# Kernel tuning notes

Measured on AMD Instinct MI355X. Metric: run time of the kernel, lower is better.

Reference implementation:

```python
import jax, jax.numpy as jnp
import numpy as np

B, P, H, D = 32, 384, 384, 512
DA, DC, DH, NUM_LABELS = 512, 512, 512, 3


def setup_inputs() -> dict:
    key = jax.random.key(0)
    ks = jax.random.split(key, 12)
    s = lambda d: 1.0 / np.sqrt(d)
    return {
        "embedded_premise": jax.random.normal(ks[0], (B, P, D), jnp.float32),
        "embedded_hypothesis": jax.random.normal(ks[1], (B, H, D), jnp.float32),
        "premise_mask": jax.random.randint(ks[2], (B, P), 0, 2, jnp.int32),
        "hypothesis_mask": jax.random.randint(ks[3], (B, H), 0, 2, jnp.int32),
        "W_attend": jax.random.normal(ks[4], (D, DA), jnp.float32) * s(D),
        "b_attend": jnp.zeros((DA,), jnp.float32),
        "W_compare": jax.random.normal(ks[5], (2 * D, DC), jnp.float32) * s(2 * D),
        "b_compare": jnp.zeros((DC,), jnp.float32),
        "W_agg1": jax.random.normal(ks[6], (2 * DC, DH), jnp.float32) * s(2 * DC),
        "b_agg1": jnp.zeros((DH,), jnp.float32),
        "W_agg2": jax.random.normal(ks[7], (DH, NUM_LABELS), jnp.float32) * s(DH),
        "b_agg2": jnp.zeros((NUM_LABELS,), jnp.float32),
    }


def masked_softmax(scores, mask):
    # AllenNLP (legacy, non-memory-efficient) masked_softmax:
    # softmax(scores * mask), re-mask, renormalize with epsilon.
    result = jax.nn.softmax(scores * mask, axis=-1)
    result = result * mask
    return result / (jnp.sum(result, axis=-1, keepdims=True) + 1e-13)


def reference(embedded_premise, embedded_hypothesis, premise_mask, hypothesis_mask,
              W_attend, b_attend, W_compare, b_compare,
              W_agg1, b_agg1, W_agg2, b_agg2):
    pm = premise_mask.astype(jnp.float32)      # [B, P]
    hm = hypothesis_mask.astype(jnp.float32)   # [B, H]

    # TimeDistributed attend feedforward (shared weights)
    proj_p = jax.nn.relu(embedded_premise @ W_attend + b_attend)      # [B, P, DA]
    proj_h = jax.nn.relu(embedded_hypothesis @ W_attend + b_attend)   # [B, H, DA]

    # Dot-product similarity matrix [B, P, H]
    sim = jnp.einsum('bpd,bhd->bph', proj_p, proj_h)

    # Cross attention with masked softmax
    p2h = masked_softmax(sim, hm[:, None, :])                          # [B, P, H]
    attended_hypothesis = jnp.einsum('bph,bhd->bpd', p2h, embedded_hypothesis)
    h2p = masked_softmax(jnp.swapaxes(sim, 1, 2), pm[:, None, :])      # [B, H, P]
    attended_premise = jnp.einsum('bhp,bpd->bhd', h2p, embedded_premise)

    # Compare feedforward on concatenated inputs, then masked sum over time
    cmp_p = jax.nn.relu(
        jnp.concatenate([embedded_premise, attended_hypothesis], axis=-1) @ W_compare + b_compare)
    compared_premise = jnp.sum(cmp_p * pm[:, :, None], axis=1)         # [B, DC]
    cmp_h = jax.nn.relu(
        jnp.concatenate([embedded_hypothesis, attended_premise], axis=-1) @ W_compare + b_compare)
    compared_hypothesis = jnp.sum(cmp_h * hm[:, :, None], axis=1)      # [B, DC]

    # Aggregate feedforward
    agg = jnp.concatenate([compared_premise, compared_hypothesis], axis=-1)
    hidden = jax.nn.relu(agg @ W_agg1 + b_agg1)
    label_logits = hidden @ W_agg2 + b_agg2                            # [B, NUM_LABELS]
    label_probs = jax.nn.softmax(label_logits, axis=-1)
    return label_logits, label_probs, h2p, p2h
```

## Files before the change

### kernel.cpp

```cpp
#include <hip/hip_runtime.h>
#include <hip/hip_bf16.h>
#include <math.h>

typedef __bf16 bf16_t;
typedef __bf16 bf16x8 __attribute__((ext_vector_type(8)));
typedef float f32x4 __attribute__((ext_vector_type(4)));

#define NPH 12288
#define SIM_B (384*384)
#define EMB_B (384*512)

#define OUT_LOGITS 0
#define OUT_PROBS 96
#define OUT_H2P 192
#define OUT_P2H (192 + 32*384*384)

#define OFF_WAT 0L
#define OFF_WCT 1048576L
#define OFF_P1  2097152L
#define OFF_P2  (OFF_P1 + 25165824L)
#define OFF_SIM (OFF_P2 + 25165824L)
#define OFF_H   (OFF_SIM + 18874368L)
#define OFF_CM  (OFF_H + 65536L)
#define OFF_CS  (OFF_CM + 49152L)
#define OFF_GP  (OFF_CS + 49152L)

#define BM 128
#define BN 128
#define BKK 32

#define M_SPLIT3 0
#define M_PLAIN  1
#define M_CONCAT 2

__device__ inline void gload16(const void* g, void* l) {
    __builtin_amdgcn_global_load_lds(
        (const __attribute__((address_space(1))) void*)g,
        (__attribute__((address_space(3))) void*)l, 16, 0, 0);
}

template<bool SPLIT>
__device__ inline void stage_tile_f32(const float* __restrict__ s,
                                      bf16_t* hi, bf16_t* lo, int eoff)
{
    float xs[16];
    *(float4*)&xs[0]  = *(const float4*)(s);
    *(float4*)&xs[4]  = *(const float4*)(s + 4);
    *(float4*)&xs[8]  = *(const float4*)(s + 8);
    *(float4*)&xs[12] = *(const float4*)(s + 12);
    bf16x8 h0, h1, l0, l1;
    #pragma unroll
    for (int i = 0; i < 8; i++) {
        float x = xs[i];     bf16_t hh = (bf16_t)x; h0[i] = hh;
        float y = xs[i + 8]; bf16_t hy = (bf16_t)y; h1[i] = hy;
        if (SPLIT) { l0[i] = (bf16_t)(x - (float)hh); l1[i] = (bf16_t)(y - (float)hy); }
    }
    *(bf16x8*)&hi[eoff]     = h0;
    *(bf16x8*)&hi[eoff + 8] = h1;
    if (SPLIT) { *(bf16x8*)&lo[eoff] = l0; *(bf16x8*)&lo[eoff + 8] = l1; }
}

template<int MODE, bool BIAS, bool RELU, bool OUTBF16>
__global__ __launch_bounds__(256) void mgemm(
    const float* __restrict__ Af, const bf16_t* __restrict__ A2b,
    const float* __restrict__ Bf, const bf16_t* __restrict__ Bb,
    const float* __restrict__ bias,
    float* __restrict__ Cf, bf16_t* __restrict__ Cb,
    int K, int K1,
    long aB, long a2B, long bB, long cB,
    int lda, int lda2, int ldb, int ldc)
{
    constexpr int NS = (MODE == M_SPLIT3) ? 2 : 1;
    __shared__ bf16_t As[NS][BM * BKK];
    __shared__ bf16_t Bs[NS][BM * BKK];

    const int tid = threadIdx.x;
    const long z = blockIdx.z;
    const int m0 = blockIdx.y * BM, n0 = blockIdx.x * BN;

    const int sr = tid >> 1, sc = (tid & 1) * 16;
    const int gr = tid >> 2, gc = (tid & 3) * 8;
    const int wlds = (tid >> 6) * 512;

    const int l = tid & 63;
    const int wv = tid >> 6;
    const int wr = (wv >> 1) * 64, wc = (wv & 1) * 64;
    const int fr = l & 15, fq = l >> 4;

    f32x4 acc[4][4] = {};

    for (int k0 = 0; k0 < K; k0 += BKK) {
        if (MODE != M_CONCAT || k0 < K1) {
            const float* s = Af + z * aB + (long)(m0 + sr) * lda + k0 + sc;
            stage_tile_f32<MODE == M_SPLIT3>(s, As[0], As[NS - 1], sr * BKK + sc);
        } else {
            const bf16_t* s = A2b + z * a2B + (long)(m0 + gr) * lda2 + (k0 - K1) + gc;
            gload16(s, &As[0][wlds]);
            gload16(s + (long)64 * lda2, &As[0][2048 + wlds]);
        }
        if (MODE == M_SPLIT3) {
            const float* s = Bf + z * bB + (long)(n0 + sr) * ldb + k0 + sc;
            stage_tile_f32<true>(s, Bs[0], Bs[NS - 1], sr * BKK + sc);
        } else {
            const bf16_t* s = Bb + z * bB + (long)(n0 + gr) * ldb + k0 + gc;
            gload16(s, &Bs[0][wlds]);
            gload16(s + (long)64 * ldb, &Bs[0][2048 + wlds]);
        }
        __syncthreads();

        bf16x8 a_h[4], b_h[4], a_l[4], b_l[4];
        #pragma unroll
        for (int i = 0; i < 4; i++) {
            a_h[i] = *(const bf16x8*)&As[0][(wr + i * 16 + fr) * BKK + fq * 8];
            b_h[i] = *(const bf16x8*)&Bs[0][(wc + i * 16 + fr) * BKK + fq * 8];
            if (MODE == M_SPLIT3) {
                a_l[i] = *(const bf16x8*)&As[NS - 1][(wr + i * 16 + fr) * BKK + fq * 8];
                b_l[i] = *(const bf16x8*)&Bs[NS - 1][(wc + i * 16 + fr) * BKK + fq * 8];
            }
        }
        #pragma unroll
        for (int mi = 0; mi < 4; mi++)
            #pragma unroll
            for (int ni = 0; ni < 4; ni++) {
                acc[mi][ni] = __builtin_amdgcn_mfma_f32_16x16x32_bf16(a_h[mi], b_h[ni], acc[mi][ni], 0, 0, 0);
                if (MODE == M_SPLIT3) {
                    acc[mi][ni] = __builtin_amdgcn_mfma_f32_16x16x32_bf16(a_h[mi], b_l[ni], acc[mi][ni], 0, 0, 0);
                    acc[mi][ni] = __builtin_amdgcn_mfma_f32_16x16x32_bf16(a_l[mi], b_h[ni], acc[mi][ni], 0, 0, 0);
                }
            }
        __syncthreads();
    }

    #pragma unroll
    for (int ni = 0; ni < 4; ni++) {
        const int col = n0 + wc + ni * 16 + fr;
        const float bv = BIAS ? bias[col] : 0.f;
        #pragma unroll
        for (int mi = 0; mi < 4; mi++) {
            #pragma unroll
            for (int j = 0; j < 4; j++) {
                const int row = m0 + wr + mi * 16 + fq * 4 + j;
                float v = acc[mi][ni][j] + bv;
                if (RELU) v = fmaxf(v, 0.f);
                if (OUTBF16) Cb[z * cB + (long)row * ldc + col] = (bf16_t)v;
                else         Cf[z * cB + (long)row * ldc + col] = v;
            }
        }
    }
}

template<typename OutT>
__global__ __launch_bounds__(256) void transpose_cvt(
    const float* __restrict__ in, OutT* __restrict__ out,
    int R, int C, long inB, long outB)
{
    __shared__ float tile[32][33];
    const long z = blockIdx.z;
    const float* src = in + z * inB;
    OutT* dst = out + z * outB;
    const int x0 = blockIdx.x * 32, y0 = blockIdx.y * 32;
    const int tx = threadIdx.x & 31, ty = threadIdx.x >> 5;
    #pragma unroll
    for (int i = 0; i < 32; i += 8)
        tile[ty + i][tx] = src[(long)(y0 + ty + i) * C + x0 + tx];
    __syncthreads();
    #pragma unroll
    for (int i = 0; i < 32; i += 8)
        dst[(long)(x0 + ty + i) * R + y0 + tx] = (OutT)tile[tx][ty + i];
}

__global__ __launch_bounds__(384) void masked_softmax_row(
    const float* __restrict__ S, const int* __restrict__ mask,
    float* __restrict__ out)
{
    const int row = blockIdx.x;
    const int b = row / 384;
    const int t = threadIdx.x;
    __shared__ float redmax[6], redsum[6];

    float v = S[(long)row * 384 + t];
    int mm = mask[b * 384 + t];

    float x = mm ? v : -3.4e38f;
    #pragma unroll
    for (int o = 32; o > 0; o >>= 1) x = fmaxf(x, __shfl_xor(x, o, 64));
    int wid = t >> 6, lane = t & 63;
    if (lane == 0) redmax[wid] = x;
    __syncthreads();
    float mx = redmax[0];
    #pragma unroll
    for (int w = 1; w < 6; w++) mx = fmaxf(mx, redmax[w]);

    float e = mm ? expf(v - mx) : 0.f;
    float s = e;
    #pragma unroll
    for (int o = 32; o > 0; o >>= 1) s += __shfl_xor(s, o, 64);
    if (lane == 0) redsum[wid] = s;
    __syncthreads();
    float tot = 0.f;
    #pragma unroll
    for (int w = 0; w < 6; w++) tot += redsum[w];

    out[(long)row * 384 + t] = (tot > 0.f) ? e / tot : 0.f;
}

__global__ __launch_bounds__(256) void col_stats(
    const float* __restrict__ S, const int* __restrict__ mask,
    float* __restrict__ cmax, float* __restrict__ csum)
{
    __shared__ int pml[384];
    __shared__ float mred[4][64], sred[4][64];
    const int b = blockIdx.y;
    const int h0 = blockIdx.x * 64;
    const int t = threadIdx.x;
    const int tk = t >> 6, hh = t & 63;

    for (int i = t; i < 384; i += 256) pml[i] = mask[b * 384 + i];
    __syncthreads();

    const float* Sb = S + (long)b * SIM_B + h0 + hh;
    float m = -3.4e38f;
    for (int p = tk; p < 384; p += 4)
        if (pml[p]) m = fmaxf(m, Sb[(long)p * 384]);
    mred[tk][hh] = m;
    __syncthreads();
    const float M = fmaxf(fmaxf(mred[0][hh], mred[1][hh]),
                          fmaxf(mred[2][hh], mred[3][hh]));
    float s = 0.f;
    for (int p = tk; p < 384; p += 4)
        if (pml[p]) s += expf(Sb[(long)p * 384] - M);
    sred[tk][hh] = s;
    __syncthreads();
    if (t < 64) {
        const float Mf = fmaxf(fmaxf(mred[0][t], mred[1][t]),
                               fmaxf(mred[2][t], mred[3][t]));
        cmax[b * 384 + h0 + t] = Mf;
        csum[b * 384 + h0 + t] = sred[0][t] + sred[1][t] + sred[2][t] + sred[3][t];
    }
}

__global__ __launch_bounds__(256) void col_write(
    const float* __restrict__ S, const int* __restrict__ mask,
    const float* __restrict__ cmax, const float* __restrict__ csum,
    float* __restrict__ out)
{
    __shared__ float tile[32][33];
    const int b = blockIdx.z;
    const int h0 = blockIdx.x * 32, p0 = blockIdx.y * 32;
    const int tx = threadIdx.x & 31, ty = threadIdx.x >> 5;
    const float* src = S + (long)b * SIM_B;
    #pragma unroll
    for (int i = 0; i < 32; i += 8)
        tile[ty + i][tx] = src[(long)(p0 + ty + i) * 384 + h0 + tx];
    __syncthreads();
    const int pm_v = mask[b * 384 + p0 + tx];
    float* dst = out + (long)b * SIM_B;
    #pragma unroll
    for (int i = 0; i < 32; i += 8) {
        const int h = h0 + ty + i;
        const float mx = cmax[b * 384 + h];
        const float tot = csum[b * 384 + h];
        float v = tile[tx][ty + i];
        float r = (pm_v && tot > 0.f) ? expf(v - mx) / tot : 0.f;
        dst[(long)h * 384 + p0 + tx] = r;
    }
}

__global__ __launch_bounds__(128) void masked_sum_kernel(
    const float* __restrict__ cmp, const int* __restrict__ mask,
    float* __restrict__ Gp, int off)
{
    const int b = blockIdx.z, pc = blockIdx.y;
    const int d = blockIdx.x * 128 + threadIdx.x;
    float acc = 0.f;
    const float* base = cmp + (long)b * EMB_B + d;
    const int* mrow = mask + b * 384;
    const int p0 = pc * 96;
    for (int p = p0; p < p0 + 96; p++)
        acc += base[(long)p * 512] * (float)mrow[p];
    Gp[((long)pc * 32 + b) * 1024 + off + d] = acc;
}

__global__ __launch_bounds__(256) void hidden_kernel(
    const float* __restrict__ Gp, const float* __restrict__ W1,
    const float* __restrict__ b1, float* __restrict__ Hbuf)
{
    __shared__ float g[1024];
    __shared__ float part[4][64];
    const int b = blockIdx.y, j0 = blockIdx.x * 64;
    const int t = threadIdx.x;
    for (int i = t; i < 1024; i += 256)
        g[i] = Gp[((long)0 * 32 + b) * 1024 + i] + Gp[((long)1 * 32 + b) * 1024 + i]
             + Gp[((long)2 * 32 + b) * 1024 + i] + Gp[((long)3 * 32 + b) * 1024 + i];
    __syncthreads();
    const int tj = t & 63, tk = t >> 6;
    const float* w = W1 + (long)(tk * 256) * 512 + j0 + tj;
    const float* gk = g + tk * 256;
    float acc = 0.f;
    #pragma unroll 8
    for (int k = 0; k < 256; k++)
        acc = fmaf(gk[k], w[(long)k * 512], acc);
    part[tk][tj] = acc;
    __syncthreads();
    if (t < 64) {
        float v = part[0][t] + part[1][t] + part[2][t] + part[3][t] + b1[j0 + t];
        Hbuf[(long)b * 512 + j0 + t] = fmaxf(v, 0.f);
    }
}

__global__ __launch_bounds__(64) void logits_kernel(
    const float* __restrict__ Hbuf, const float* __restrict__ W2,
    const float* __restrict__ b2, float* __restrict__ out)
{
    const int b = blockIdx.x, l = threadIdx.x;
    const float* h = Hbuf + (long)b * 512;
    float a0 = 0.f, a1 = 0.f, a2 = 0.f;
    #pragma unroll
    for (int k = l; k < 512; k += 64) {
        float hv = h[k];
        a0 = fmaf(hv, W2[k * 3 + 0], a0);
        a1 = fmaf(hv, W2[k * 3 + 1], a1);
        a2 = fmaf(hv, W2[k * 3 + 2], a2);
    }
    #pragma unroll
    for (int o = 32; o > 0; o >>= 1) {
        a0 += __shfl_xor(a0, o, 64);
        a1 += __shfl_xor(a1, o, 64);
        a2 += __shfl_xor(a2, o, 64);
    }
    if (l == 0) {
        float l0 = a0 + b2[0], l1 = a1 + b2[1], l2 = a2 + b2[2];
        float mx = fmaxf(l0, fmaxf(l1, l2));
        float e0 = expf(l0 - mx), e1 = expf(l1 - mx), e2 = expf(l2 - mx);
        float s = e0 + e1 + e2;
        out[OUT_LOGITS + b * 3 + 0] = l0;
        out[OUT_LOGITS + b * 3 + 1] = l1;
        out[OUT_LOGITS + b * 3 + 2] = l2;
        out[OUT_PROBS + b * 3 + 0] = e0 / s;
        out[OUT_PROBS + b * 3 + 1] = e1 / s;
        out[OUT_PROBS + b * 3 + 2] = e2 / s;
    }
}

extern "C" void kernel_launch(void* const* d_in, const int* in_sizes, int n_in,
                              void* d_out, int out_size, void* d_ws, size_t ws_size,
                              hipStream_t stream) {
    const float* emb_p = (const float*)d_in[0];
    const float* emb_h = (const float*)d_in[1];
    const int* pm = (const int*)d_in[2];
    const int* hm = (const int*)d_in[3];
    const float* Wa = (const float*)d_in[4];
    const float* ba = (const float*)d_in[5];
    const float* Wc = (const float*)d_in[6];
    const float* bc = (const float*)d_in[7];
    const float* W1 = (const float*)d_in[8];
    const float* b1 = (const float*)d_in[9];
    const float* W2 = (const float*)d_in[10];
    const float* b2 = (const float*)d_in[11];
    float* out = (float*)d_out;
    char* W = (char*)d_ws;

    float*  WaT   = (float*)(W + OFF_WAT);
    bf16_t* WcT   = (bf16_t*)(W + OFF_WCT);
    float*  projp = (float*)(W + OFF_P1);
    float*  projh = (float*)(W + OFF_P2);
    float*  sim   = (float*)(W + OFF_SIM);
    float*  Hbuf  = (float*)(W + OFF_H);
    float*  cmaxb = (float*)(W + OFF_CM);
    float*  csumb = (float*)(W + OFF_CS);
    float*  Gp    = (float*)(W + OFF_GP);
    bf16_t* atth  = (bf16_t*)(W + OFF_P1);
    bf16_t* attp  = (bf16_t*)(W + OFF_P1 + 12582912L);
    bf16_t* embTp = (bf16_t*)(W + OFF_P2);
    bf16_t* embTh = (bf16_t*)(W + OFF_P2 + 12582912L);
    float*  cmp   = (float*)(W + OFF_P2);

    transpose_cvt<float><<<dim3(16, 16, 1), 256, 0, stream>>>(Wa, WaT, 512, 512, 0, 0);
    transpose_cvt<bf16_t><<<dim3(16, 32, 1), 256, 0, stream>>>(Wc, WcT, 1024, 512, 0, 0);

    mgemm<M_SPLIT3, true, true, false><<<dim3(4, 96, 1), 256, 0, stream>>>(
        emb_p, nullptr, WaT, nullptr, ba, projp, nullptr,
        512, 0, 0, 0, 0, 0, 512, 0, 512, 512);
    mgemm<M_SPLIT3, true, true, false><<<dim3(4, 96, 1), 256, 0, stream>>>(
        emb_h, nullptr, WaT, nullptr, ba, projh, nullptr,
        512, 0, 0, 0, 0, 0, 512, 0, 512, 512);

    mgemm<M_SPLIT3, false, false, false><<<dim3(3, 3, 32), 256, 0, stream>>>(
        projp, nullptr, projh, nullptr, nullptr, sim, nullptr,
        512, 0, EMB_B, 0, EMB_B, SIM_B, 512, 0, 512, 384);

    masked_softmax_row<<<NPH, 384, 0, stream>>>(sim, hm, out + OUT_P2H);
    col_stats<<<dim3(6, 32), 256, 0, stream>>>(sim, pm, cmaxb, csumb);
    col_write<<<dim3(12, 12, 32), 256, 0, stream>>>(sim, pm, cmaxb, csumb, out + OUT_H2P);

    transpose_cvt<bf16_t><<<dim3(16, 12, 32), 256, 0, stream>>>(emb_p, embTp, 384, 512, EMB_B, EMB_B);
    transpose_cvt<bf16_t><<<dim3(16, 12, 32), 256, 0, stream>>>(emb_h, embTh, 384, 512, EMB_B, EMB_B);

    mgemm<M_PLAIN, false, false, true><<<dim3(4, 3, 32), 256, 0, stream>>>(
        out + OUT_P2H, nullptr, nullptr, embTh, nullptr, nullptr, atth,
        384, 0, SIM_B, 0, (long)512 * 384, EMB_B, 384, 0, 384, 512);
    mgemm<M_PLAIN, false, false, true><<<dim3(4, 3, 32), 256, 0, stream>>>(
        out + OUT_H2P, nullptr, nullptr, embTp, nullptr, nullptr, attp,
        384, 0, SIM_B, 0, (long)512 * 384, EMB_B, 384, 0, 384, 512);

    mgemm<M_CONCAT, true, true, false><<<dim3(4, 96, 1), 256, 0, stream>>>(
        emb_p, atth, nullptr, WcT, bc, cmp, nullptr,
        1024, 512, 0, 0, 0, 0, 512, 512, 1024, 512);
    masked_sum_kernel<<<dim3(4, 4, 32), 128, 0, stream>>>(cmp, pm, Gp, 0);

    mgemm<M_CONCAT, true, true, false><<<dim3(4, 96, 1), 256, 0, stream>>>(
        emb_h, attp, nullptr, WcT, bc, cmp, nullptr,
        1024, 512, 0, 0, 0, 0, 512, 512, 1024, 512);
    masked_sum_kernel<<<dim3(4, 4, 32), 128, 0, stream>>>(cmp, hm, Gp, 512);

    hidden_kernel<<<dim3(8, 32), 256, 0, stream>>>(Gp, W1, b1, Hbuf);
    logits_kernel<<<32, 64, 0, stream>>>(Hbuf, W2, b2, out);
}
```

Before: 452.2 us.

## Store split-bf16 intermediates, swizzle LDS, and batch paired GEMMs into single launches

The projection GEMM now writes its output as hi/lo bf16 pairs instead of fp32. The similarity GEMM then loads both operands straight into LDS with async global_load_lds, with no per-tile fp32 conversion. LDS tiles use an XOR swizzle to cut bank conflicts. Premise/hypothesis GEMMs, transposes and masked sums are merged into single launches along the z dimension, and the compare output is stored as bf16. The aim is less memory traffic, less conversion work and fewer launches, at the cost of more pointer arithmetic and a small precision change in the compare output.

Measured after the change: 407.3 us. 1.11x faster.

```diff
diff --git a/kernel.cpp b/kernel.cpp
--- a/kernel.cpp
+++ b/kernel.cpp
@@ -15,23 +15,32 @@
 #define OUT_H2P 192
 #define OUT_P2H (192 + 32*384*384)
 
-#define OFF_WAT 0L
-#define OFF_WCT 1048576L
-#define OFF_P1  2097152L
-#define OFF_P2  (OFF_P1 + 25165824L)
-#define OFF_SIM (OFF_P2 + 25165824L)
-#define OFF_H   (OFF_SIM + 18874368L)
-#define OFF_CM  (OFF_H + 65536L)
-#define OFF_CS  (OFF_CM + 49152L)
-#define OFF_GP  (OFF_CS + 49152L)
+#define OFF_WATH 0L
+#define OFF_WATL 524288L
+#define OFF_WCT  1048576L
+#define OFF_A    2097152L
+#define OFF_SIM  52428800L
+#define OFF_CM   71303168L
+#define OFF_CS   (OFF_CM + 49152L)
+#define OFF_GP   (OFF_CS + 49152L)
+#define OFF_H    (OFF_GP + 524288L)
+
+#define PROJ_LO   6291456L
+#define PROJ_Z    12582912L
+#define ATT_ALL_E 12582912L
+#define CMP_Z     6291456L
 
 #define BM 128
 #define BN 128
 #define BKK 32
 
-#define M_SPLIT3 0
-#define M_PLAIN  1
-#define M_CONCAT 2
+#define M_PROJ   0
+#define M_SPLITB 1
+#define M_PLAIN  2
+#define M_CONCAT 3
+#define O_F32   0
+#define O_BF16  1
+#define O_SPLIT 2
 
 __device__ inline void gload16(const void* g, void* l) {
     __builtin_amdgcn_global_load_lds(
@@ -40,8 +49,8 @@
 }
 
 template<bool SPLIT>
-__device__ inline void stage_tile_f32(const float* __restrict__ s,
-                                      bf16_t* hi, bf16_t* lo, int eoff)
+__device__ inline void stage_sw(const float* __restrict__ s,
+                                bf16_t* hi, bf16_t* lo, int row, int c0)
 {
     float xs[16];
     *(float4*)&xs[0]  = *(const float4*)(s);
@@ -55,22 +64,29 @@
         float y = xs[i + 8]; bf16_t hy = (bf16_t)y; h1[i] = hy;
         if (SPLIT) { l0[i] = (bf16_t)(x - (float)hh); l1[i] = (bf16_t)(y - (float)hy); }
     }
-    *(bf16x8*)&hi[eoff]     = h0;
-    *(bf16x8*)&hi[eoff + 8] = h1;
-    if (SPLIT) { *(bf16x8*)&lo[eoff] = l0; *(bf16x8*)&lo[eoff + 8] = l1; }
-}
-
-template<int MODE, bool BIAS, bool RELU, bool OUTBF16>
+    const int key = (row >> 1) & 3;
+    const int cc0 = c0 ^ key, cc1 = cc0 ^ 1;
+    *(bf16x8*)&hi[row * 32 + cc0 * 8] = h0;
+    *(bf16x8*)&hi[row * 32 + cc1 * 8] = h1;
+    if (SPLIT) {
+        *(bf16x8*)&lo[row * 32 + cc0 * 8] = l0;
+        *(bf16x8*)&lo[row * 32 + cc1 * 8] = l1;
+    }
+}
+
+template<int MODE, int OUTK, bool BIAS, bool RELU>
 __global__ __launch_bounds__(256) void mgemm(
-    const float* __restrict__ Af, const bf16_t* __restrict__ A2b,
-    const float* __restrict__ Bf, const bf16_t* __restrict__ Bb,
+    const float* __restrict__ Af, const float* __restrict__ Af2, int zalt,
+    const bf16_t* __restrict__ Abh, long loA,
+    const bf16_t* __restrict__ A2b, long a2B,
+    const bf16_t* __restrict__ Bbh, long loB,
     const float* __restrict__ bias,
-    float* __restrict__ Cf, bf16_t* __restrict__ Cb,
+    float* __restrict__ Cf, bf16_t* __restrict__ Cb, long loC,
     int K, int K1,
-    long aB, long a2B, long bB, long cB,
+    long aB, long bB, long cB,
     int lda, int lda2, int ldb, int ldc)
 {
-    constexpr int NS = (MODE == M_SPLIT3) ? 2 : 1;
+    constexpr int NS = (MODE == M_PROJ || MODE == M_SPLITB) ? 2 : 1;
     __shared__ bf16_t As[NS][BM * BKK];
     __shared__ bf16_t Bs[NS][BM * BKK];
 
@@ -78,8 +94,12 @@
     const long z = blockIdx.z;
     const int m0 = blockIdx.y * BM, n0 = blockIdx.x * BN;
 
-    const int sr = tid >> 1, sc = (tid & 1) * 16;
-    const int gr = tid >> 2, gc = (tid & 3) * 8;
+    const float* Afs = (MODE == M_PROJ || MODE == M_PLAIN || MODE == M_CONCAT)
+                       ? ((z >= zalt) ? Af2 : Af) : nullptr;
+
+    const int sr = tid >> 1, sc = (tid & 1) * 16, c0 = (tid & 1) * 2;
+    const int gr = tid >> 2;
+    const int gco = ((tid & 3) ^ ((gr >> 1) & 3)) * 8;
     const int wlds = (tid >> 6) * 512;
 
     const int l = tid & 63;
@@ -90,32 +110,48 @@
     f32x4 acc[4][4] = {};
 
     for (int k0 = 0; k0 < K; k0 += BKK) {
-        if (MODE != M_CONCAT || k0 < K1) {
-            const float* s = Af + z * aB + (long)(m0 + sr) * lda + k0 + sc;
-            stage_tile_f32<MODE == M_SPLIT3>(s, As[0], As[NS - 1], sr * BKK + sc);
+        if (MODE == M_PROJ || MODE == M_PLAIN) {
+            const float* s = Afs + z * aB + (long)(m0 + sr) * lda + k0 + sc;
+            stage_sw<MODE == M_PROJ>(s, As[0], As[NS - 1], sr, c0);
+        } else if (MODE == M_CONCAT) {
+            if (k0 < K1) {
+                const float* s = Afs + z * aB + (long)(m0 + sr) * lda + k0 + sc;
+                stage_sw<false>(s, As[0], nullptr, sr, c0);
+            } else {
+                const bf16_t* s = A2b + z * a2B + (long)(m0 + gr) * lda2 + (k0 - K1) + gco;
+                gload16(s, &As[0][wlds]);
+                gload16(s + (long)64 * lda2, &As[0][2048 + wlds]);
+            }
         } else {
-            const bf16_t* s = A2b + z * a2B + (long)(m0 + gr) * lda2 + (k0 - K1) + gc;
+            const bf16_t* s = Abh + z * aB + (long)(m0 + gr) * lda + k0 + gco;
             gload16(s, &As[0][wlds]);
-            gload16(s + (long)64 * lda2, &As[0][2048 + wlds]);
+            gload16(s + (long)64 * lda, &As[0][2048 + wlds]);
+            gload16(s + loA, &As[NS - 1][wlds]);
+            gload16(s + loA + (long)64 * lda, &As[NS - 1][2048 + wlds]);
         }
-        if (MODE == M_SPLIT3) {
-            const float* s = Bf + z * bB + (long)(n0 + sr) * ldb + k0 + sc;
-            stage_tile_f32<true>(s, Bs[0], Bs[NS - 1], sr * BKK + sc);
-        } else {
-            const bf16_t* s = Bb + z * bB + (long)(n0 + gr) * ldb + k0 + gc;
+        {
+            const bf16_t* s = Bbh + z * bB + (long)(n0 + gr) * ldb + k0 + gco;
             gload16(s, &Bs[0][wlds]);
             gload16(s + (long)64 * ldb, &Bs[0][2048 + wlds]);
+            if (NS == 2) {
+                gload16(s + loB, &Bs[NS - 1][wlds]);
+                gload16(s + loB + (long)64 * ldb, &Bs[NS - 1][2048 + wlds]);
+            }
         }
         __syncthreads();
 
         bf16x8 a_h[4], b_h[4], a_l[4], b_l[4];
         #pragma unroll
         for (int i = 0; i < 4; i++) {
-            a_h[i] = *(const bf16x8*)&As[0][(wr + i * 16 + fr) * BKK + fq * 8];
-            b_h[i] = *(const bf16x8*)&Bs[0][(wc + i * 16 + fr) * BKK + fq * 8];
-            if (MODE == M_SPLIT3) {
-                a_l[i] = *(const bf16x8*)&As[NS - 1][(wr + i * 16 + fr) * BKK + fq * 8];
-                b_l[i] = *(const bf16x8*)&Bs[NS - 1][(wc + i * 16 + fr) * BKK + fq * 8];
+            const int ra = wr + i * 16 + fr;
+            const int rb = wc + i * 16 + fr;
+            const int ka = (fq ^ ((ra >> 1) & 3)) * 8;
+            const int kb = (fq ^ ((rb >> 1) & 3)) * 8;
+            a_h[i] = *(const bf16x8*)&As[0][ra * 32 + ka];
+            b_h[i] = *(const bf16x8*)&Bs[0][rb * 32 + kb];
+            if (NS == 2) {
+                a_l[i] = *(const bf16x8*)&As[NS - 1][ra * 32 + ka];
+                b_l[i] = *(const bf16x8*)&Bs[NS - 1][rb * 32 + kb];
             }
         }
         #pragma unroll
@@ -123,7 +159,7 @@
             #pragma unroll
             for (int ni = 0; ni < 4; ni++) {
                 acc[mi][ni] = __builtin_amdgcn_mfma_f32_16x16x32_bf16(a_h[mi], b_h[ni], acc[mi][ni], 0, 0, 0);
-                if (MODE == M_SPLIT3) {
+                if (NS == 2) {
                     acc[mi][ni] = __builtin_amdgcn_mfma_f32_16x16x32_bf16(a_h[mi], b_l[ni], acc[mi][ni], 0, 0, 0);
                     acc[mi][ni] = __builtin_amdgcn_mfma_f32_16x16x32_bf16(a_l[mi], b_h[ni], acc[mi][ni], 0, 0, 0);
                 }
@@ -142,31 +178,44 @@
                 const int row = m0 + wr + mi * 16 + fq * 4 + j;
                 float v = acc[mi][ni][j] + bv;
                 if (RELU) v = fmaxf(v, 0.f);
-                if (OUTBF16) Cb[z * cB + (long)row * ldc + col] = (bf16_t)v;
-                else         Cf[z * cB + (long)row * ldc + col] = v;
+                const long idx = z * cB + (long)row * ldc + col;
+                if (OUTK == O_F32) Cf[idx] = v;
+                else if (OUTK == O_BF16) Cb[idx] = (bf16_t)v;
+                else {
+                    bf16_t h = (bf16_t)v;
+                    Cb[idx] = h;
+                    Cb[idx + loC] = (bf16_t)(v - (float)h);
+                }
             }
         }
     }
 }
 
-template<typename OutT>
-__global__ __launch_bounds__(256) void transpose_cvt(
-    const float* __restrict__ in, OutT* __restrict__ out,
+template<bool SPLIT>
+__global__ __launch_bounds__(256) void transpose_kernel(
+    const float* __restrict__ in, const float* __restrict__ in2, int zsplit,
+    bf16_t* __restrict__ out, bf16_t* __restrict__ outLo,
     int R, int C, long inB, long outB)
 {
     __shared__ float tile[32][33];
-    const long z = blockIdx.z;
-    const float* src = in + z * inB;
-    OutT* dst = out + z * outB;
+    const int z = blockIdx.z;
+    const float* src = (z >= zsplit) ? (in2 + (long)(z - zsplit) * inB)
+                                     : (in + (long)z * inB);
     const int x0 = blockIdx.x * 32, y0 = blockIdx.y * 32;
     const int tx = threadIdx.x & 31, ty = threadIdx.x >> 5;
     #pragma unroll
     for (int i = 0; i < 32; i += 8)
         tile[ty + i][tx] = src[(long)(y0 + ty + i) * C + x0 + tx];
     __syncthreads();
-    #pragma unroll
-    for (int i = 0; i < 32; i += 8)
-        dst[(long)(x0 + ty + i) * R + y0 + tx] = (OutT)tile[tx][ty + i];
+    bf16_t* dst = out + (long)z * outB;
+    bf16_t* dstL = SPLIT ? (outLo + (long)z * outB) : nullptr;
+    #pragma unroll
+    for (int i = 0; i < 32; i += 8) {
+        float v = tile[tx][ty + i];
+        bf16_t h = (bf16_t)v;
+        dst[(long)(x0 + ty + i) * R + y0 + tx] = h;
+        if (SPLIT) dstL[(long)(x0 + ty + i) * R + y0 + tx] = (bf16_t)(v - (float)h);
+    }
 }
 
 __global__ __launch_bounds__(384) void masked_softmax_row(
@@ -267,18 +316,19 @@
 }
 
 __global__ __launch_bounds__(128) void masked_sum_kernel(
-    const float* __restrict__ cmp, const int* __restrict__ mask,
-    float* __restrict__ Gp, int off)
-{
-    const int b = blockIdx.z, pc = blockIdx.y;
+    const bf16_t* __restrict__ cmpb, const int* __restrict__ pm,
+    const int* __restrict__ hm, float* __restrict__ Gp)
+{
+    const int b = blockIdx.z;
+    const int pc = blockIdx.y & 3, half = blockIdx.y >> 2;
     const int d = blockIdx.x * 128 + threadIdx.x;
+    const int* mrow = (half ? hm : pm) + b * 384;
+    const bf16_t* base = cmpb + (long)half * CMP_Z + (long)b * EMB_B + d;
     float acc = 0.f;
-    const float* base = cmp + (long)b * EMB_B + d;
-    const int* mrow = mask + b * 384;
     const int p0 = pc * 96;
     for (int p = p0; p < p0 + 96; p++)
-        acc += base[(long)p * 512] * (float)mrow[p];
-    Gp[((long)pc * 32 + b) * 1024 + off + d] = acc;
+        acc += (float)base[(long)p * 512] * (float)mrow[p];
+    Gp[((long)pc * 32 + b) * 1024 + half * 512 + d] = acc;
 }
 
 __global__ __launch_bounds__(256) void hidden_kernel(
@@ -360,58 +410,57 @@
     float* out = (float*)d_out;
     char* W = (char*)d_ws;
 
-    float*  WaT   = (float*)(W + OFF_WAT);
+    bf16_t* WaTh  = (bf16_t*)(W + OFF_WATH);
+    bf16_t* WaTl  = (bf16_t*)(W + OFF_WATL);
     bf16_t* WcT   = (bf16_t*)(W + OFF_WCT);
-    float*  projp = (float*)(W + OFF_P1);
-    float*  projh = (float*)(W + OFF_P2);
+    bf16_t* A     = (bf16_t*)(W + OFF_A);
     float*  sim   = (float*)(W + OFF_SIM);
-    float*  Hbuf  = (float*)(W + OFF_H);
     float*  cmaxb = (float*)(W + OFF_CM);
     float*  csumb = (float*)(W + OFF_CS);
     float*  Gp    = (float*)(W + OFF_GP);
-    bf16_t* atth  = (bf16_t*)(W + OFF_P1);
-    bf16_t* attp  = (bf16_t*)(W + OFF_P1 + 12582912L);
-    bf16_t* embTp = (bf16_t*)(W + OFF_P2);
-    bf16_t* embTh = (bf16_t*)(W + OFF_P2 + 12582912L);
-    float*  cmp   = (float*)(W + OFF_P2);
-
-    transpose_cvt<float><<<dim3(16, 16, 1), 256, 0, stream>>>(Wa, WaT, 512, 512, 0, 0);
-    transpose_cvt<bf16_t><<<dim3(16, 32, 1), 256, 0, stream>>>(Wc, WcT, 1024, 512, 0, 0);
-
-    mgemm<M_SPLIT3, true, true, false><<<dim3(4, 96, 1), 256, 0, stream>>>(
-        emb_p, nullptr, WaT, nullptr, ba, projp, nullptr,
-        512, 0, 0, 0, 0, 0, 512, 0, 512, 512);
-    mgemm<M_SPLIT3, true, true, false><<<dim3(4, 96, 1), 256, 0, stream>>>(
-        emb_h, nullptr, WaT, nullptr, ba, projh, nullptr,
-        512, 0, 0, 0, 0, 0, 512, 0, 512, 512);
-
-    mgemm<M_SPLIT3, false, false, false><<<dim3(3, 3, 32), 256, 0, stream>>>(
-        projp, nullptr, projh, nullptr, nullptr, sim, nullptr,
-        512, 0, EMB_B, 0, EMB_B, SIM_B, 512, 0, 512, 384);
+    float*  Hbuf  = (float*)(W + OFF_H);
+    bf16_t* projs  = A;
+    bf16_t* embT   = A;
+    bf16_t* attAll = A + ATT_ALL_E;
+    bf16_t* cmpAll = A;
+
+    transpose_kernel<true><<<dim3(16, 16, 1), 256, 0, stream>>>(
+        Wa, nullptr, 999, WaTh, WaTl, 512, 512, 0, 0);
+    transpose_kernel<false><<<dim3(16, 32, 1), 256, 0, stream>>>(
+        Wc, nullptr, 999, WcT, nullptr, 1024, 512, 0, 0);
+
+    mgemm<M_PROJ, O_SPLIT, true, true><<<dim3(4, 96, 2), 256, 0, stream>>>(
+        emb_p, emb_h, 1, nullptr, 0, nullptr, 0, WaTh, 262144L, ba,
+        nullptr, projs, PROJ_LO,
+        512, 0, 0L, 0L, PROJ_Z, 512, 0, 512, 512);
+
+    mgemm<M_SPLITB, O_F32, false, false><<<dim3(3, 3, 32), 256, 0, stream>>>(
+        nullptr, nullptr, 999, projs, PROJ_LO, nullptr, 0,
+        projs + PROJ_Z, PROJ_LO, nullptr,
+        sim, nullptr, 0,
+        512, 0, (long)EMB_B, (long)EMB_B, (long)SIM_B, 512, 0, 512, 384);
 
     masked_softmax_row<<<NPH, 384, 0, stream>>>(sim, hm, out + OUT_P2H);
     col_stats<<<dim3(6, 32), 256, 0, stream>>>(sim, pm, cmaxb, csumb);
     col_write<<<dim3(12, 12, 32), 256, 0, stream>>>(sim, pm, cmaxb, csumb, out + OUT_H2P);
 
-    transpose_cvt<bf16_t><<<dim3(16, 12, 32), 256, 0, stream>>>(emb_p, embTp, 384, 512, EMB_B, EMB_B);
-    transpose_cvt<bf16_t><<<dim3(16, 12, 32), 256, 0, stream>>>(emb_h, embTh, 384, 512, EMB_B, EMB_B);
-
-    mgemm<M_PLAIN, false, false, true><<<dim3(4, 3, 32), 256, 0, stream>>>(
-        out + OUT_P2H, nullptr, nullptr, embTh, nullptr, nullptr, atth,
-        384, 0, SIM_B, 0, (long)512 * 384, EMB_B, 384, 0, 384, 512);
-    mgemm<M_PLAIN, false, false, true><<<dim3(4, 3, 32), 256, 0, stream>>>(
-        out + OUT_H2P, nullptr, nullptr, embTp, nullptr, nullptr, attp,
-        384, 0, SIM_B, 0, (long)512 * 384, EMB_B, 384, 0, 384, 512);
-
-    mgemm<M_CONCAT, true, true, false><<<dim3(4, 96, 1), 256, 0, stream>>>(
-        emb_p, atth, nullptr, WcT, bc, cmp, nullptr,
-        1024, 512, 0, 0, 0, 0, 512, 512, 1024, 512);
-    masked_sum_kernel<<<dim3(4, 4, 32), 128, 0, stream>>>(cmp, pm, Gp, 0);
-
-    mgemm<M_CONCAT, true, true, false><<<dim3(4, 96, 1), 256, 0, stream>>>(
-        emb_h, attp, nullptr, WcT, bc, cmp, nullptr,
-        1024, 512, 0, 0, 0, 0, 512, 512, 1024, 512);
-    masked_sum_kernel<<<dim3(4, 4, 32), 128, 0, stream>>>(cmp, hm, Gp, 512);
+    transpose_kernel<false><<<dim3(16, 12, 64), 256, 0, stream>>>(
+        emb_p, emb_h, 32, embT, nullptr, 384, 512, (long)EMB_B, (long)EMB_B);
+
+    mgemm<M_PLAIN, O_BF16, false, false><<<dim3(4, 3, 64), 256, 0, stream>>>(
+        out + OUT_H2P, nullptr, 1 << 30, nullptr, 0, nullptr, 0,
+        embT, 0, nullptr,
+        nullptr, attAll, 0,
+        384, 0, (long)SIM_B, (long)EMB_B, (long)EMB_B, 384, 0, 384, 512);
+
+    mgemm<M_CONCAT, O_BF16, true, true><<<dim3(4, 96, 2), 256, 0, stream>>>(
+        emb_p, emb_h, 1, nullptr, 0,
+        attAll + CMP_Z, -(long)CMP_Z,
+        WcT, 0, bc,
+        nullptr, cmpAll, 0,
+        1024, 512, 0L, 0L, (long)CMP_Z, 512, 512, 1024, 512);
+
+    masked_sum_kernel<<<dim3(4, 8, 32), 128, 0, stream>>>(cmpAll, pm, hm, Gp);
 
     hidden_kernel<<<dim3(8, 32), 256, 0, stream>>>(Gp, W1, b1, Hbuf);
     logits_kernel<<<32, 64, 0, stream>>>(Hbuf, W2, b2, out);
```
